# Performance work log

Measured on AMD Instinct MI355X. Metric: run time of the kernel, lower is better.

The kernel has to match this reference:

```python
import jax, jax.numpy as jnp
import numpy as np


@jax.custom_vjp
def sign_ste(x):
    return jnp.sign(x)

def _sign_ste_fwd(x):
    return jnp.sign(x), x

def _sign_ste_bwd(x, g):
    gate = (jnp.abs(x) < 1.0).astype(g.dtype)
    return (g * gate,)

sign_ste.defvjp(_sign_ste_fwd, _sign_ste_bwd)


def setup_inputs() -> dict:
    key = jax.random.key(0)
    ks = jax.random.split(key, 6)
    B, S, D_IN, D_OUT, R = 4, 4096, 4096, 4096, 128
    x = jax.random.normal(ks[0], (B, S, D_IN), dtype=jnp.float32)
    U_latent = jax.random.normal(ks[1], (D_OUT, R), dtype=jnp.float32) * 0.05
    V_latent = jax.random.normal(ks[2], (D_IN, R), dtype=jnp.float32) * 0.05
    s1 = jax.random.uniform(ks[3], (D_OUT,), dtype=jnp.float32, minval=0.01, maxval=0.1)
    s2 = jax.random.uniform(ks[4], (D_IN,), dtype=jnp.float32, minval=0.01, maxval=0.1)
    bias = jax.random.normal(ks[5], (D_OUT,), dtype=jnp.float32) * 0.02
    return {"x": x, "U_latent": U_latent, "V_latent": V_latent, "s1": s1, "s2": s2, "bias": bias}


def reference(x, U_latent, V_latent, s1, s2, bias):
    cdtype = x.dtype
    U_sign = sign_ste(U_latent.astype(cdtype))  # [d_out, r]
    V_sign = sign_ste(V_latent.astype(cdtype))  # [d_in, r]
    z = x * s2.astype(cdtype)                   # [..., d_in]
    z = z @ V_sign                               # [..., r]
    z = z @ U_sign.T                             # [..., d_out]
    z = z * s1.astype(cdtype)
    z = z + bias.astype(cdtype)
    return z
```

## Files before the change

### kernel.cpp

```cpp
#include <hip/hip_runtime.h>

typedef float f32x4 __attribute__((ext_vector_type(4)));
typedef short s16x8 __attribute__((ext_vector_type(8)));
typedef short s16x4 __attribute__((ext_vector_type(4)));

#define M_TOT 16384
#define K_IN  4096
#define R_DIM 128
#define N_OUT 4096

__device__ __forceinline__ short sign_bf16(float v) {
  return v > 0.f ? (short)0x3F80 : (v < 0.f ? (short)0xBF80 : (short)0);
}

__device__ __forceinline__ void f32_to_bf16_pair(float f, short& h, short& l) {
  unsigned u = __float_as_uint(f);
  unsigned r = u + 0x7fffu + ((u >> 16) & 1u);
  h = (short)(r >> 16);
  float fh = __uint_as_float(r & 0xffff0000u);
  float fl = f - fh;
  unsigned u2 = __float_as_uint(fl);
  unsigned r2 = u2 + 0x7fffu + ((u2 >> 16) & 1u);
  l = (short)(r2 >> 16);
}

__global__ __launch_bounds__(256)
void k_prep(const float* __restrict__ U, const float* __restrict__ V,
            short* __restrict__ VsT, short* __restrict__ Us) {
  int i = blockIdx.x * 256 + threadIdx.x;
  if (i < R_DIM * K_IN) {
    int n = i >> 12;
    int k = i & 4095;
    VsT[i] = sign_bf16(V[(size_t)k * R_DIM + n]);
    Us[i]  = sign_bf16(U[i]);
  }
}

__global__ __launch_bounds__(512, 4)
void k1_z(const float* __restrict__ x, const float* __restrict__ s2,
          const short* __restrict__ VsT, float* __restrict__ Z) {
  __shared__ short Ahi[32 * 64];
  __shared__ short Alo[32 * 64];
  __shared__ short Bt[128 * 64];

  const int t = threadIdx.x;
  const int lane = t & 63;
  const int wave = t >> 6;
  const int m0 = blockIdx.x * 32;

  const int sr = t >> 4;
  const int sk = (t & 15) * 4;
  const float* xrow = x + (size_t)(m0 + sr) * K_IN + sk;
  const int aoff = sr * 128 + (((t & 15) * 8) ^ ((sr & 7) << 4));

  const int bn = t >> 2;
  const int bkb = (t & 3) * 32;
  const char* vrow = (const char*)VsT + (size_t)bn * (K_IN * 2) + bkb;
  const int bsw = (bn & 7) << 4;
  const int boff0 = bn * 128 + (bkb ^ bsw);
  const int boff1 = bn * 128 + ((bkb + 16) ^ bsw);

  const int mg = wave & 1;
  const int nq = wave >> 1;
  const int fr = mg * 16 + (lane & 15);
  const int rsw = (lane & 7) << 4;
  const int kgrp = (lane >> 4) * 16;
  const int bn0 = nq * 32 + (lane & 15);
  const int bn1 = bn0 + 16;

  f32x4 acc0 = {0.f, 0.f, 0.f, 0.f};
  f32x4 acc1 = {0.f, 0.f, 0.f, 0.f};

  f32x4 xa = *(const f32x4*)xrow;
  f32x4 sa = *(const f32x4*)(s2 + sk);
  s16x8 v0 = *(const s16x8*)(vrow);
  s16x8 v1 = *(const s16x8*)(vrow + 16);

  for (int kt = 0; kt < 64; ++kt) {
    __syncthreads();
    {
      s16x4 h4, l4;
#pragma unroll
      for (int j = 0; j < 4; ++j) {
        float f = xa[j] * sa[j];
        short hh, ll;
        f32_to_bf16_pair(f, hh, ll);
        h4[j] = hh; l4[j] = ll;
      }
      *(s16x4*)((char*)Ahi + aoff) = h4;
      *(s16x4*)((char*)Alo + aoff) = l4;
      *(s16x8*)((char*)Bt + boff0) = v0;
      *(s16x8*)((char*)Bt + boff1) = v1;
    }
    __syncthreads();
    const int ktn = (kt + 1) & 63;
    f32x4 xan = *(const f32x4*)(xrow + ktn * 64);
    f32x4 san = *(const f32x4*)(s2 + ktn * 64 + sk);
    s16x8 v0n = *(const s16x8*)(vrow + ktn * 128);
    s16x8 v1n = *(const s16x8*)(vrow + ktn * 128 + 16);
#pragma unroll
    for (int ks = 0; ks < 2; ++ks) {
      const int kb = ks * 64 + kgrp;
      s16x8 ah = *(const s16x8*)((const char*)Ahi + fr * 128 + (kb ^ rsw));
      s16x8 al = *(const s16x8*)((const char*)Alo + fr * 128 + (kb ^ rsw));
      s16x8 b0 = *(const s16x8*)((const char*)Bt + bn0 * 128 + (kb ^ rsw));
      s16x8 b1 = *(const s16x8*)((const char*)Bt + bn1 * 128 + (kb ^ rsw));
      acc0 = __builtin_amdgcn_mfma_f32_16x16x32_bf16(ah, b0, acc0, 0, 0, 0);
      acc0 = __builtin_amdgcn_mfma_f32_16x16x32_bf16(al, b0, acc0, 0, 0, 0);
      acc1 = __builtin_amdgcn_mfma_f32_16x16x32_bf16(ah, b1, acc1, 0, 0, 0);
      acc1 = __builtin_amdgcn_mfma_f32_16x16x32_bf16(al, b1, acc1, 0, 0, 0);
    }
    xa = xan; sa = san; v0 = v0n; v1 = v1n;
  }

  const int col0 = nq * 32 + (lane & 15);
  const int rowb = m0 + mg * 16 + (lane >> 4) * 4;
#pragma unroll
  for (int j = 0; j < 4; ++j) {
    Z[(size_t)(rowb + j) * R_DIM + col0]      = acc0[j];
    Z[(size_t)(rowb + j) * R_DIM + col0 + 16] = acc1[j];
  }
}

__global__ __launch_bounds__(512, 4)
void k2_out(const float* __restrict__ Z, const short* __restrict__ Us,
            const float* __restrict__ s1, const float* __restrict__ bias,
            float* __restrict__ out) {
  __shared__ short Zhi[128 * 128];
  __shared__ short Zlo[128 * 128];

  const int t = threadIdx.x;
  const int lane = t & 63;
  const int wave = t >> 6;
  const int bid = blockIdx.x;
  const int nb = bid & 15;
  const int mb = bid >> 4;
  const int m0 = mb * 128, n0 = nb * 256;
  const int wm = wave & 1, wn = wave >> 1;

  s16x8 bf[4][4];
#pragma unroll
  for (int ks = 0; ks < 4; ++ks) {
#pragma unroll
    for (int nf = 0; nf < 4; ++nf) {
      const int n = n0 + wn * 64 + nf * 16 + (lane & 15);
      bf[ks][nf] = *(const s16x8*)(Us + (size_t)n * R_DIM + ks * 32 + (lane >> 4) * 8);
    }
  }

  {
    const int sr = t >> 2;
    const int skf = (t & 3) * 32;
    const float* zrow = Z + (size_t)(m0 + sr) * R_DIM + skf;
    const int swr = (sr & 7) << 4;
#pragma unroll
    for (int q = 0; q < 4; ++q) {
      f32x4 a = *(const f32x4*)(zrow + q * 8);
      f32x4 b = *(const f32x4*)(zrow + q * 8 + 4);
      s16x8 h, l;
#pragma unroll
      for (int j = 0; j < 4; ++j) {
        short hh, ll;
        f32_to_bf16_pair(a[j], hh, ll); h[j] = hh;     l[j] = ll;
        f32_to_bf16_pair(b[j], hh, ll); h[j + 4] = hh; l[j + 4] = ll;
      }
      const int off = sr * 256 + ((((t & 3) * 64) + q * 16) ^ swr);
      *(s16x8*)((char*)Zhi + off) = h;
      *(s16x8*)((char*)Zlo + off) = l;
    }
  }
  __syncthreads();

  f32x4 acc[4][4] = {};
  const int rsw = (lane & 7) << 4;
  const int kg = (lane >> 4) * 16;
#pragma unroll
  for (int mf = 0; mf < 4; ++mf) {
    const int r = wm * 64 + mf * 16 + (lane & 15);
    const int rbase = r * 256;
#pragma unroll
    for (int ks = 0; ks < 4; ++ks) {
      const int kb = ks * 64 + kg;
      s16x8 ah = *(const s16x8*)((const char*)Zhi + rbase + (kb ^ rsw));
      s16x8 al = *(const s16x8*)((const char*)Zlo + rbase + (kb ^ rsw));
#pragma unroll
      for (int nf = 0; nf < 4; ++nf) {
        acc[mf][nf] = __builtin_amdgcn_mfma_f32_16x16x32_bf16(ah, bf[ks][nf], acc[mf][nf], 0, 0, 0);
        acc[mf][nf] = __builtin_amdgcn_mfma_f32_16x16x32_bf16(al, bf[ks][nf], acc[mf][nf], 0, 0, 0);
      }
    }
  }

#pragma unroll
  for (int nf = 0; nf < 4; ++nf) {
    const int col = n0 + wn * 64 + nf * 16 + (lane & 15);
    const float sv = s1[col];
    const float bv = bias[col];
#pragma unroll
    for (int mf = 0; mf < 4; ++mf) {
      const int row = m0 + wm * 64 + mf * 16 + (lane >> 4) * 4;
#pragma unroll
      for (int j = 0; j < 4; ++j) {
        out[(size_t)(row + j) * N_OUT + col] = acc[mf][nf][j] * sv + bv;
      }
    }
  }
}

extern "C" void kernel_launch(void* const* d_in, const int* in_sizes, int n_in,
                              void* d_out, int out_size, void* d_ws, size_t ws_size,
                              hipStream_t stream) {
  const float* x    = (const float*)d_in[0];
  const float* U    = (const float*)d_in[1];
  const float* V    = (const float*)d_in[2];
  const float* s1   = (const float*)d_in[3];
  const float* s2   = (const float*)d_in[4];
  const float* bias = (const float*)d_in[5];
  float* out = (float*)d_out;

  short* VsT = (short*)d_ws;
  short* Us  = VsT + R_DIM * K_IN;
  float* Z   = (float*)(Us + N_OUT * R_DIM);

  k_prep<<<dim3(2048), dim3(256), 0, stream>>>(U, V, VsT, Us);
  k1_z<<<dim3(512), dim3(512), 0, stream>>>(x, s2, VsT, Z);
  k2_out<<<dim3(2048), dim3(512), 0, stream>>>(Z, Us, s1, bias, out);
}
```

Baseline: 579.5 us.

## Rewrite low-rank path with fp16 split MFMA, split-K stage one, smaller output tiles

Moves both GEMM stages from a bf16 hi/lo split to an fp16 hi/lo split. Stage one becomes a wave-per-16-rows, split-K-by-two kernel that reads B fragments straight from global memory with no shared-memory staging or barriers, writing two partial Z buffers. Stage two sums the partials while converting to fp16 and uses 128x128 output tiles instead of 128x256, doubling the grid. The prep kernel now transposes V through shared memory with vector stores. The aim is to cut the barrier and LDS cost in the x-streaming stage and raise parallelism, at the cost of extra Z traffic and a possible precision change from fp16 range limits.

```diff
diff --git a/kernel.cpp b/kernel.cpp
--- a/kernel.cpp
+++ b/kernel.cpp
@@ -1,177 +1,185 @@
 #include <hip/hip_runtime.h>
 
 typedef float f32x4 __attribute__((ext_vector_type(4)));
-typedef short s16x8 __attribute__((ext_vector_type(8)));
-typedef short s16x4 __attribute__((ext_vector_type(4)));
+typedef _Float16 f16x8 __attribute__((ext_vector_type(8)));
+typedef _Float16 f16x4 __attribute__((ext_vector_type(4)));
 
 #define M_TOT 16384
 #define K_IN  4096
 #define R_DIM 128
 #define N_OUT 4096
 
-__device__ __forceinline__ short sign_bf16(float v) {
-  return v > 0.f ? (short)0x3F80 : (v < 0.f ? (short)0xBF80 : (short)0);
-}
-
-__device__ __forceinline__ void f32_to_bf16_pair(float f, short& h, short& l) {
-  unsigned u = __float_as_uint(f);
-  unsigned r = u + 0x7fffu + ((u >> 16) & 1u);
-  h = (short)(r >> 16);
-  float fh = __uint_as_float(r & 0xffff0000u);
-  float fl = f - fh;
-  unsigned u2 = __float_as_uint(fl);
-  unsigned r2 = u2 + 0x7fffu + ((u2 >> 16) & 1u);
-  l = (short)(r2 >> 16);
+__device__ __forceinline__ _Float16 sign_f16(float v) {
+  return v > 0.f ? (_Float16)1.f : (v < 0.f ? (_Float16)-1.f : (_Float16)0.f);
 }
 
 __global__ __launch_bounds__(256)
 void k_prep(const float* __restrict__ U, const float* __restrict__ V,
-            short* __restrict__ VsT, short* __restrict__ Us) {
-  int i = blockIdx.x * 256 + threadIdx.x;
-  if (i < R_DIM * K_IN) {
-    int n = i >> 12;
-    int k = i & 4095;
-    VsT[i] = sign_bf16(V[(size_t)k * R_DIM + n]);
-    Us[i]  = sign_bf16(U[i]);
-  }
-}
-
-__global__ __launch_bounds__(512, 4)
+            _Float16* __restrict__ VsT, _Float16* __restrict__ Us) {
+  __shared__ _Float16 tl[128 * 36];
+  const int t = threadIdx.x;
+  const int b = blockIdx.x;
+  const int k0 = b * 32;
+
+#pragma unroll
+  for (int e = 0; e < 16; ++e) {
+    int idx = e * 256 + t;
+    int k = idx >> 7;
+    int r = idx & 127;
+    tl[r * 36 + k] = sign_f16(V[(size_t)(k0 + k) * R_DIM + r]);
+  }
+  __syncthreads();
+
+  {
+    const int r = t >> 1;
+    const int kh = (t & 1) * 16;
+    f16x8 o0, o1;
+#pragma unroll
+    for (int j = 0; j < 8; ++j) {
+      o0[j] = tl[r * 36 + kh + j];
+      o1[j] = tl[r * 36 + kh + 8 + j];
+    }
+    *(f16x8*)(VsT + (size_t)r * K_IN + k0 + kh) = o0;
+    *(f16x8*)(VsT + (size_t)r * K_IN + k0 + kh + 8) = o1;
+  }
+
+#pragma unroll
+  for (int e = 0; e < 4; ++e) {
+    size_t base = (size_t)b * 4096 + (size_t)e * 1024 + (size_t)t * 4;
+    f32x4 u = *(const f32x4*)(U + base);
+    f16x4 s;
+#pragma unroll
+    for (int j = 0; j < 4; ++j) s[j] = sign_f16(u[j]);
+    *(f16x4*)(Us + base) = s;
+  }
+}
+
+__global__ __launch_bounds__(256, 2)
 void k1_z(const float* __restrict__ x, const float* __restrict__ s2,
-          const short* __restrict__ VsT, float* __restrict__ Z) {
-  __shared__ short Ahi[32 * 64];
-  __shared__ short Alo[32 * 64];
-  __shared__ short Bt[128 * 64];
-
+          const _Float16* __restrict__ VsT, float* __restrict__ Z2) {
   const int t = threadIdx.x;
   const int lane = t & 63;
   const int wave = t >> 6;
-  const int m0 = blockIdx.x * 32;
-
-  const int sr = t >> 4;
-  const int sk = (t & 15) * 4;
-  const float* xrow = x + (size_t)(m0 + sr) * K_IN + sk;
-  const int aoff = sr * 128 + (((t & 15) * 8) ^ ((sr & 7) << 4));
-
-  const int bn = t >> 2;
-  const int bkb = (t & 3) * 32;
-  const char* vrow = (const char*)VsT + (size_t)bn * (K_IN * 2) + bkb;
-  const int bsw = (bn & 7) << 4;
-  const int boff0 = bn * 128 + (bkb ^ bsw);
-  const int boff1 = bn * 128 + ((bkb + 16) ^ bsw);
-
-  const int mg = wave & 1;
-  const int nq = wave >> 1;
-  const int fr = mg * 16 + (lane & 15);
-  const int rsw = (lane & 7) << 4;
-  const int kgrp = (lane >> 4) * 16;
-  const int bn0 = nq * 32 + (lane & 15);
-  const int bn1 = bn0 + 16;
-
-  f32x4 acc0 = {0.f, 0.f, 0.f, 0.f};
-  f32x4 acc1 = {0.f, 0.f, 0.f, 0.f};
-
-  f32x4 xa = *(const f32x4*)xrow;
-  f32x4 sa = *(const f32x4*)(s2 + sk);
-  s16x8 v0 = *(const s16x8*)(vrow);
-  s16x8 v1 = *(const s16x8*)(vrow + 16);
-
-  for (int kt = 0; kt < 64; ++kt) {
-    __syncthreads();
-    {
-      s16x4 h4, l4;
-#pragma unroll
-      for (int j = 0; j < 4; ++j) {
-        float f = xa[j] * sa[j];
-        short hh, ll;
-        f32_to_bf16_pair(f, hh, ll);
-        h4[j] = hh; l4[j] = ll;
-      }
-      *(s16x4*)((char*)Ahi + aoff) = h4;
-      *(s16x4*)((char*)Alo + aoff) = l4;
-      *(s16x8*)((char*)Bt + boff0) = v0;
-      *(s16x8*)((char*)Bt + boff1) = v1;
-    }
-    __syncthreads();
-    const int ktn = (kt + 1) & 63;
-    f32x4 xan = *(const f32x4*)(xrow + ktn * 64);
-    f32x4 san = *(const f32x4*)(s2 + ktn * 64 + sk);
-    s16x8 v0n = *(const s16x8*)(vrow + ktn * 128);
-    s16x8 v1n = *(const s16x8*)(vrow + ktn * 128 + 16);
-#pragma unroll
-    for (int ks = 0; ks < 2; ++ks) {
-      const int kb = ks * 64 + kgrp;
-      s16x8 ah = *(const s16x8*)((const char*)Ahi + fr * 128 + (kb ^ rsw));
-      s16x8 al = *(const s16x8*)((const char*)Alo + fr * 128 + (kb ^ rsw));
-      s16x8 b0 = *(const s16x8*)((const char*)Bt + bn0 * 128 + (kb ^ rsw));
-      s16x8 b1 = *(const s16x8*)((const char*)Bt + bn1 * 128 + (kb ^ rsw));
-      acc0 = __builtin_amdgcn_mfma_f32_16x16x32_bf16(ah, b0, acc0, 0, 0, 0);
-      acc0 = __builtin_amdgcn_mfma_f32_16x16x32_bf16(al, b0, acc0, 0, 0, 0);
-      acc1 = __builtin_amdgcn_mfma_f32_16x16x32_bf16(ah, b1, acc1, 0, 0, 0);
-      acc1 = __builtin_amdgcn_mfma_f32_16x16x32_bf16(al, b1, acc1, 0, 0, 0);
-    }
-    xa = xan; sa = san; v0 = v0n; v1 = v1n;
-  }
-
-  const int col0 = nq * 32 + (lane & 15);
-  const int rowb = m0 + mg * 16 + (lane >> 4) * 4;
-#pragma unroll
-  for (int j = 0; j < 4; ++j) {
-    Z[(size_t)(rowb + j) * R_DIM + col0]      = acc0[j];
-    Z[(size_t)(rowb + j) * R_DIM + col0 + 16] = acc1[j];
+  const int wid = blockIdx.x * 4 + wave;
+  const int half = wid & 1;
+  const int g = wid >> 1;
+  const int m0 = g * 16;
+  const int k0 = half * 2048;
+  const int row = lane & 15;
+  const int kq = (lane >> 4) * 8;
+
+  const float* xp = x + (size_t)(m0 + row) * K_IN + k0 + kq;
+  const float* sp = s2 + k0 + kq;
+  const _Float16* bp = VsT + (size_t)row * K_IN + k0 + kq;
+
+  f32x4 acc[8];
+#pragma unroll
+  for (int i = 0; i < 8; ++i) acc[i] = (f32x4){0.f, 0.f, 0.f, 0.f};
+
+  f32x4 xa0 = *(const f32x4*)xp;
+  f32x4 xa1 = *(const f32x4*)(xp + 4);
+  f32x4 sa0 = *(const f32x4*)sp;
+  f32x4 sa1 = *(const f32x4*)(sp + 4);
+
+  for (int st = 0; st < 64; ++st) {
+    f16x8 bfr[8];
+#pragma unroll
+    for (int nf = 0; nf < 8; ++nf)
+      bfr[nf] = *(const f16x8*)(bp + (size_t)nf * 16 * K_IN + st * 32);
+
+    f16x8 ah, al;
+#pragma unroll
+    for (int j = 0; j < 4; ++j) {
+      float f0 = xa0[j] * sa0[j];
+      float f1 = xa1[j] * sa1[j];
+      _Float16 h0 = (_Float16)f0;
+      _Float16 h1 = (_Float16)f1;
+      ah[j] = h0;
+      ah[j + 4] = h1;
+      al[j] = (_Float16)(f0 - (float)h0);
+      al[j + 4] = (_Float16)(f1 - (float)h1);
+    }
+
+    const int sn = (st + 1) & 63;
+    xa0 = *(const f32x4*)(xp + sn * 32);
+    xa1 = *(const f32x4*)(xp + sn * 32 + 4);
+    sa0 = *(const f32x4*)(sp + sn * 32);
+    sa1 = *(const f32x4*)(sp + sn * 32 + 4);
+
+#pragma unroll
+    for (int nf = 0; nf < 8; ++nf) {
+      acc[nf] = __builtin_amdgcn_mfma_f32_16x16x32_f16(ah, bfr[nf], acc[nf], 0, 0, 0);
+      acc[nf] = __builtin_amdgcn_mfma_f32_16x16x32_f16(al, bfr[nf], acc[nf], 0, 0, 0);
+    }
+  }
+
+  float* Zp = Z2 + (size_t)half * M_TOT * R_DIM;
+  const int rw = m0 + (lane >> 4) * 4;
+#pragma unroll
+  for (int nf = 0; nf < 8; ++nf) {
+    const int col = nf * 16 + row;
+#pragma unroll
+    for (int j = 0; j < 4; ++j)
+      Zp[(size_t)(rw + j) * R_DIM + col] = acc[nf][j];
   }
 }
 
 __global__ __launch_bounds__(512, 4)
-void k2_out(const float* __restrict__ Z, const short* __restrict__ Us,
+void k2_out(const float* __restrict__ Z2, const _Float16* __restrict__ Us,
             const float* __restrict__ s1, const float* __restrict__ bias,
             float* __restrict__ out) {
-  __shared__ short Zhi[128 * 128];
-  __shared__ short Zlo[128 * 128];
+  __shared__ _Float16 Zhi[128 * 128];
+  __shared__ _Float16 Zlo[128 * 128];
 
   const int t = threadIdx.x;
   const int lane = t & 63;
   const int wave = t >> 6;
   const int bid = blockIdx.x;
-  const int nb = bid & 15;
-  const int mb = bid >> 4;
-  const int m0 = mb * 128, n0 = nb * 256;
+  const int nb = bid & 31;
+  const int mb = bid >> 5;
+  const int m0 = mb * 128, n0 = nb * 128;
   const int wm = wave & 1, wn = wave >> 1;
 
-  s16x8 bf[4][4];
-#pragma unroll
-  for (int ks = 0; ks < 4; ++ks) {
-#pragma unroll
-    for (int nf = 0; nf < 4; ++nf) {
-      const int n = n0 + wn * 64 + nf * 16 + (lane & 15);
-      bf[ks][nf] = *(const s16x8*)(Us + (size_t)n * R_DIM + ks * 32 + (lane >> 4) * 8);
-    }
-  }
+  f16x8 bf[4][2];
+#pragma unroll
+  for (int ks = 0; ks < 4; ++ks)
+#pragma unroll
+    for (int nf = 0; nf < 2; ++nf) {
+      const int n = n0 + wn * 32 + nf * 16 + (lane & 15);
+      bf[ks][nf] = *(const f16x8*)(Us + (size_t)n * R_DIM + ks * 32 + (lane >> 4) * 8);
+    }
 
   {
     const int sr = t >> 2;
     const int skf = (t & 3) * 32;
-    const float* zrow = Z + (size_t)(m0 + sr) * R_DIM + skf;
+    const float* za = Z2 + (size_t)(m0 + sr) * R_DIM + skf;
+    const float* zb = za + (size_t)M_TOT * R_DIM;
     const int swr = (sr & 7) << 4;
 #pragma unroll
     for (int q = 0; q < 4; ++q) {
-      f32x4 a = *(const f32x4*)(zrow + q * 8);
-      f32x4 b = *(const f32x4*)(zrow + q * 8 + 4);
-      s16x8 h, l;
+      f32x4 a0 = *(const f32x4*)(za + q * 8);
+      f32x4 a1 = *(const f32x4*)(za + q * 8 + 4);
+      f32x4 b0 = *(const f32x4*)(zb + q * 8);
+      f32x4 b1 = *(const f32x4*)(zb + q * 8 + 4);
+      f16x8 h, l;
 #pragma unroll
       for (int j = 0; j < 4; ++j) {
-        short hh, ll;
-        f32_to_bf16_pair(a[j], hh, ll); h[j] = hh;     l[j] = ll;
-        f32_to_bf16_pair(b[j], hh, ll); h[j + 4] = hh; l[j + 4] = ll;
+        float f0 = a0[j] + b0[j];
+        float f1 = a1[j] + b1[j];
+        _Float16 h0 = (_Float16)f0, h1 = (_Float16)f1;
+        h[j] = h0;
+        h[j + 4] = h1;
+        l[j] = (_Float16)(f0 - (float)h0);
+        l[j + 4] = (_Float16)(f1 - (float)h1);
       }
       const int off = sr * 256 + ((((t & 3) * 64) + q * 16) ^ swr);
-      *(s16x8*)((char*)Zhi + off) = h;
-      *(s16x8*)((char*)Zlo + off) = l;
+      *(f16x8*)((char*)Zhi + off) = h;
+      *(f16x8*)((char*)Zlo + off) = l;
     }
   }
   __syncthreads();
 
-  f32x4 acc[4][4] = {};
+  f32x4 acc[4][2] = {};
   const int rsw = (lane & 7) << 4;
   const int kg = (lane >> 4) * 16;
 #pragma unroll
@@ -181,28 +189,27 @@
 #pragma unroll
     for (int ks = 0; ks < 4; ++ks) {
       const int kb = ks * 64 + kg;
-      s16x8 ah = *(const s16x8*)((const char*)Zhi + rbase + (kb ^ rsw));
-      s16x8 al = *(const s16x8*)((const char*)Zlo + rbase + (kb ^ rsw));
-#pragma unroll
-      for (int nf = 0; nf < 4; ++nf) {
-        acc[mf][nf] = __builtin_amdgcn_mfma_f32_16x16x32_bf16(ah, bf[ks][nf], acc[mf][nf], 0, 0, 0);
-        acc[mf][nf] = __builtin_amdgcn_mfma_f32_16x16x32_bf16(al, bf[ks][nf], acc[mf][nf], 0, 0, 0);
+      f16x8 ah = *(const f16x8*)((const char*)Zhi + rbase + (kb ^ rsw));
+      f16x8 al = *(const f16x8*)((const char*)Zlo + rbase + (kb ^ rsw));
+#pragma unroll
+      for (int nf = 0; nf < 2; ++nf) {
+        acc[mf][nf] = __builtin_amdgcn_mfma_f32_16x16x32_f16(ah, bf[ks][nf], acc[mf][nf], 0, 0, 0);
+        acc[mf][nf] = __builtin_amdgcn_mfma_f32_16x16x32_f16(al, bf[ks][nf], acc[mf][nf], 0, 0, 0);
       }
     }
   }
 
 #pragma unroll
-  for (int nf = 0; nf < 4; ++nf) {
-    const int col = n0 + wn * 64 + nf * 16 + (lane & 15);
+  for (int nf = 0; nf < 2; ++nf) {
+    const int col = n0 + wn * 32 + nf * 16 + (lane & 15);
     const float sv = s1[col];
     const float bv = bias[col];
 #pragma unroll
     for (int mf = 0; mf < 4; ++mf) {
-      const int row = m0 + wm * 64 + mf * 16 + (lane >> 4) * 4;
-#pragma unroll
-      for (int j = 0; j < 4; ++j) {
-        out[(size_t)(row + j) * N_OUT + col] = acc[mf][nf][j] * sv + bv;
-      }
+      const int row2 = m0 + wm * 64 + mf * 16 + (lane >> 4) * 4;
+#pragma unroll
+      for (int j = 0; j < 4; ++j)
+        out[(size_t)(row2 + j) * N_OUT + col] = acc[mf][nf][j] * sv + bv;
     }
   }
 }
@@ -218,11 +225,11 @@
   const float* bias = (const float*)d_in[5];
   float* out = (float*)d_out;
 
-  short* VsT = (short*)d_ws;
-  short* Us  = VsT + R_DIM * K_IN;
-  float* Z   = (float*)(Us + N_OUT * R_DIM);
-
-  k_prep<<<dim3(2048), dim3(256), 0, stream>>>(U, V, VsT, Us);
-  k1_z<<<dim3(512), dim3(512), 0, stream>>>(x, s2, VsT, Z);
-  k2_out<<<dim3(2048), dim3(512), 0, stream>>>(Z, Us, s1, bias, out);
-}
+  _Float16* VsT = (_Float16*)d_ws;
+  _Float16* Us  = VsT + (size_t)R_DIM * K_IN;
+  float*    Z2  = (float*)(Us + (size_t)N_OUT * R_DIM);
+
+  k_prep<<<dim3(128), dim3(256), 0, stream>>>(U, V, VsT, Us);
+  k1_z<<<dim3(512), dim3(256), 0, stream>>>(x, s2, VsT, Z2);
+  k2_out<<<dim3(4096), dim3(512), 0, stream>>>(Z2, Us, s1, bias, out);
+}
```

New measurement: 637.3 us. 10.0% more time.
